# Kernel optimization log

Measured on AMD Instinct MI355X. Metric: run time of the kernel, lower is better.

Reference implementation:

```python
import jax, jax.numpy as jnp
import numpy as np

I = 1739   # input/output feature size (num_nodes)
H = 256    # hidden size
T = 2048   # trajectory length


def gru(x_seq, h0, W_ih, W_hh, b_ih, b_hh):
    """PyTorch-convention GRU over x_seq [T, I] with h0 [H]. Returns (hs [T,H], h_T [H])."""
    x_proj = x_seq @ W_ih.T + b_ih  # [T, 3H], precompute input projections

    def step(h, xp):
        hh = h @ W_hh.T + b_hh  # [3H]
        xr, xz, xn = xp[:H], xp[H:2 * H], xp[2 * H:]
        hr, hz, hn = hh[:H], hh[H:2 * H], hh[2 * H:]
        r = jax.nn.sigmoid(xr + hr)
        z = jax.nn.sigmoid(xz + hz)
        n = jnp.tanh(xn + r * hn)
        h_new = (1.0 - z) * n + z * h
        return h_new, h_new

    h_T, hs = jax.lax.scan(step, h0, x_proj)
    return hs, h_T


def setup_inputs() -> dict:
    key = jax.random.key(0)
    ks = jax.random.split(key, 12)
    s = 1.0 / np.sqrt(H)
    inp = {
        "input_trajectory": jax.random.normal(ks[0], (1, T, I), jnp.float32),
        "target_trajectory": jax.random.normal(ks[1], (1, T, I), jnp.float32),
        "W_ih_enc": jax.random.uniform(ks[2], (3 * H, I), jnp.float32, -s, s),
        "W_hh_enc": jax.random.uniform(ks[3], (3 * H, H), jnp.float32, -s, s),
        "b_ih_enc": jax.random.uniform(ks[4], (3 * H,), jnp.float32, -s, s),
        "b_hh_enc": jax.random.uniform(ks[5], (3 * H,), jnp.float32, -s, s),
        "W_ih_dec": jax.random.uniform(ks[6], (3 * H, I), jnp.float32, -s, s),
        "W_hh_dec": jax.random.uniform(ks[7], (3 * H, H), jnp.float32, -s, s),
        "b_ih_dec": jax.random.uniform(ks[8], (3 * H,), jnp.float32, -s, s),
        "b_hh_dec": jax.random.uniform(ks[9], (3 * H,), jnp.float32, -s, s),
        "W_out": jax.random.uniform(ks[10], (I, H), jnp.float32, -s, s),
        "b_out": jax.random.uniform(ks[11], (I,), jnp.float32, -s, s),
    }
    return inp


def reference(input_trajectory, target_trajectory,
              W_ih_enc, W_hh_enc, b_ih_enc, b_hh_enc,
              W_ih_dec, W_hh_dec, b_ih_dec, b_hh_dec,
              W_out, b_out):
    x = input_trajectory[0]  # [T, I], batch=1
    h0 = jnp.zeros((H,), x.dtype)
    # Encoder: only the final hidden state is used.
    _, h_enc = gru(x, h0, W_ih_enc, W_hh_enc, b_ih_enc, b_hh_enc)
    # Decoder: loop feeds each input timestep through a 1-step GRU;
    # this is exactly a GRU over the full sequence starting from h_enc.
    hs, _ = gru(x, h_enc, W_ih_dec, W_hh_dec, b_ih_dec, b_hh_dec)  # [T, H]
    # Per-step Linear is a single batched matmul over all steps.
    preds = hs @ W_out.T + b_out  # [T, I]
    # Original cats per-step (1,1,I) tensors along dim=0 -> [T, 1, I].
    return preds[:, None, :]
```

## Files before the change

kernel.cpp:

```cpp
#include <hip/hip_runtime.h>
#include <hip/hip_fp16.h>

#define TT 2048
#define II 1739
#define HN 256
#define H3 768

typedef _Float16 h2 __attribute__((ext_vector_type(2)));

__device__ __forceinline__ float fdot2(h2 a, h2 b, float c) {
#if defined(__has_builtin)
#if __has_builtin(__builtin_amdgcn_fdot2)
  return __builtin_amdgcn_fdot2(a, b, c, false);
#else
  return fmaf((float)a[0], (float)b[0], fmaf((float)a[1], (float)b[1], c));
#endif
#else
  return fmaf((float)a[0], (float)b[0], fmaf((float)a[1], (float)b[1], c));
#endif
}

template <int CTRL>
__device__ __forceinline__ float dpp_qperm(float v) {
  int r = __builtin_amdgcn_update_dpp(0, __builtin_bit_cast(int, v), CTRL, 0xF, 0xF, true);
  return __builtin_bit_cast(float, r);
}

__global__ __launch_bounds__(256) void gemm_abt(
    const float* __restrict__ A, int M, int K,
    const float* __restrict__ B, int N,
    const float* __restrict__ bias1, const float* __restrict__ bias2, int b2lim,
    float* __restrict__ C) {
  __shared__ float As[16][64];
  __shared__ float Bs[16][64];
  const int tid = threadIdx.x;
  const int m0 = blockIdx.y * 64, n0 = blockIdx.x * 64;
  const int lr = tid >> 2;
  const int lk = (tid & 3) * 4;
  const int cx = tid & 15, cy = tid >> 4;
  float acc[4][4] = {};

  for (int k0 = 0; k0 < K; k0 += 16) {
#pragma unroll
    for (int i = 0; i < 4; ++i) {
      int k = k0 + lk + i;
      As[lk + i][lr] = (k < K) ? A[(size_t)(m0 + lr) * K + k] : 0.f;
      int bn = n0 + lr;
      Bs[lk + i][lr] = (k < K && bn < N) ? B[(size_t)bn * K + k] : 0.f;
    }
    __syncthreads();
#pragma unroll
    for (int k = 0; k < 16; ++k) {
      float4 av = *(const float4*)&As[k][cy * 4];
      float4 bv = *(const float4*)&Bs[k][cx * 4];
      const float aa[4] = {av.x, av.y, av.z, av.w};
      const float bb[4] = {bv.x, bv.y, bv.z, bv.w};
#pragma unroll
      for (int i = 0; i < 4; ++i)
#pragma unroll
        for (int j = 0; j < 4; ++j) acc[i][j] = fmaf(aa[i], bb[j], acc[i][j]);
    }
    __syncthreads();
  }
#pragma unroll
  for (int i = 0; i < 4; ++i) {
    int m = m0 + cy * 4 + i;
#pragma unroll
    for (int j = 0; j < 4; ++j) {
      int n = n0 + cx * 4 + j;
      if (n < N) {
        float b = bias1 ? bias1[n] : 0.f;
        if (bias2 && n < b2lim) b += bias2[n];
        C[(size_t)m * N + n] = acc[i][j] + b;
      }
    }
  }
}

__global__ __launch_bounds__(512) void gru_seq(
    const float* __restrict__ xp,
    const float* __restrict__ Whh,
    const float* __restrict__ bhh,
    const float* __restrict__ h0,
    float* __restrict__ hs_out,
    float* __restrict__ hT_out) {
  __shared__ uint4 hbuf[32];
  __shared__ float hh[H3];

  const int tid = threadIdx.x;
  const int lane = tid & 63;
  const int wv = tid >> 6;
  const int kc = lane & 3;
  const int g = wv * 16 + (lane >> 2);
  const int r0 = g * 6;

  h2 wreg[6][32];
#pragma unroll
  for (int i = 0; i < 6; ++i) {
    const float* wr = Whh + (size_t)(r0 + i) * HN + kc * 64;
#pragma unroll
    for (int p = 0; p < 32; ++p) {
      float2 f = *(const float2*)(wr + 2 * p);
      wreg[i][p] = h2{(_Float16)f.x, (_Float16)f.y};
    }
  }

  float hj = 0.f, bhn = 0.f;
  if (tid < HN) {
    hj = h0 ? h0[tid] : 0.f;
    bhn = bhh[2 * HN + tid];
  }
  if (tid < 128) {
    float a = h0 ? h0[2 * tid] : 0.f;
    float b = h0 ? h0[2 * tid + 1] : 0.f;
    ((h2*)hbuf)[tid] = h2{(_Float16)a, (_Float16)b};
  }
  __syncthreads();

  for (int t = 0; t < TT; ++t) {
    float xr = 0.f, xz = 0.f, xn = 0.f;
    if (tid < HN) {
      const float* xpt = xp + (size_t)t * H3 + tid;
      xr = xpt[0];
      xz = xpt[HN];
      xn = xpt[2 * HN];
    }

    float acc[6] = {0.f, 0.f, 0.f, 0.f, 0.f, 0.f};
#pragma unroll
    for (int hf = 0; hf < 2; ++hf) {
      uint4 v0 = hbuf[kc * 8 + hf * 4 + 0];
      uint4 v1 = hbuf[kc * 8 + hf * 4 + 1];
      uint4 v2 = hbuf[kc * 8 + hf * 4 + 2];
      uint4 v3 = hbuf[kc * 8 + hf * 4 + 3];
      uint hw[16] = {v0.x, v0.y, v0.z, v0.w, v1.x, v1.y, v1.z, v1.w,
                     v2.x, v2.y, v2.z, v2.w, v3.x, v3.y, v3.z, v3.w};
#pragma unroll
      for (int i = 0; i < 6; ++i)
#pragma unroll
        for (int p = 0; p < 16; ++p)
          acc[i] = fdot2(wreg[i][hf * 16 + p], __builtin_bit_cast(h2, hw[p]), acc[i]);
    }

#pragma unroll
    for (int i = 0; i < 6; ++i) {
      float v = acc[i];
      v += dpp_qperm<0xB1>(v);
      v += dpp_qperm<0x4E>(v);
      acc[i] = v;
    }
    if (kc == 0) {
      *(float2*)&hh[r0 + 0] = make_float2(acc[0], acc[1]);
      *(float2*)&hh[r0 + 2] = make_float2(acc[2], acc[3]);
      *(float2*)&hh[r0 + 4] = make_float2(acc[4], acc[5]);
    }
    __syncthreads();

    if (tid < HN) {
      float r = 1.f / (1.f + __expf(-(xr + hh[tid])));
      float z = 1.f / (1.f + __expf(-(xz + hh[HN + tid])));
      float nv = 2.f / (1.f + __expf(-2.f * (xn + r * (hh[2 * HN + tid] + bhn)))) - 1.f;
      hj = (1.f - z) * nv + z * hj;
      if (hs_out) hs_out[(size_t)t * HN + tid] = hj;
      ((_Float16*)hbuf)[tid] = (_Float16)hj;
    }
    __syncthreads();
  }
  if (hT_out && tid < HN) hT_out[tid] = hj;
}

extern "C" void kernel_launch(void* const* d_in, const int* in_sizes, int n_in,
                              void* d_out, int out_size, void* d_ws, size_t ws_size,
                              hipStream_t stream) {
  const float* x     = (const float*)d_in[0];
  const float* Wih_e = (const float*)d_in[2];
  const float* Whh_e = (const float*)d_in[3];
  const float* bih_e = (const float*)d_in[4];
  const float* bhh_e = (const float*)d_in[5];
  const float* Wih_d = (const float*)d_in[6];
  const float* Whh_d = (const float*)d_in[7];
  const float* bih_d = (const float*)d_in[8];
  const float* bhh_d = (const float*)d_in[9];
  const float* Wout  = (const float*)d_in[10];
  const float* bout  = (const float*)d_in[11];
  float* out = (float*)d_out;

  float* ws = (float*)d_ws;
  float* xpe  = ws;
  float* xpd  = xpe + (size_t)TT * H3;
  float* hs   = xpd + (size_t)TT * H3;
  float* henc = hs + (size_t)TT * HN;

  dim3 blk(256);
  gemm_abt<<<dim3(12, 32), blk, 0, stream>>>(x, TT, II, Wih_e, H3, bih_e, bhh_e, 2 * HN, xpe);
  gemm_abt<<<dim3(12, 32), blk, 0, stream>>>(x, TT, II, Wih_d, H3, bih_d, bhh_d, 2 * HN, xpd);
  gru_seq<<<1, 512, 0, stream>>>(xpe, Whh_e, bhh_e, nullptr, nullptr, henc);
  gru_seq<<<1, 512, 0, stream>>>(xpd, Whh_d, bhh_d, henc, hs, nullptr);
  gemm_abt<<<dim3(28, 32), blk, 0, stream>>>(hs, TT, HN, Wout, II, bout, nullptr, 0, out);
}
```

Before: 5.527 ms.

## Fuse GRU gate math into dot-product threads with double-buffered h and one barrier

Each quad of lanes now owns two hidden units across all three gates, so the gate nonlinearities run right after the DPP reduction. This removes the shared hh buffer and one of the two barriers per timestep. The hidden-state buffer is double-buffered and padded to cut bank conflicts. The log2(e) scaling is folded into the input-projection GEMM and the recurrent weights so the gates can use raw exp2/rcp intrinsics. The cost is that fp16 weights now carry scaled values and more threads do redundant gate math.

```diff
diff --git a/kernel.cpp b/kernel.cpp
--- a/kernel.cpp
+++ b/kernel.cpp
@@ -5,6 +5,7 @@
 #define II 1739
 #define HN 256
 #define H3 768
+#define L2E 1.44269504088896f
 
 typedef _Float16 h2 __attribute__((ext_vector_type(2)));
 
@@ -20,6 +21,30 @@
 #endif
 }
 
+__device__ __forceinline__ float fast_exp2(float x) {
+#if defined(__has_builtin)
+#if __has_builtin(__builtin_amdgcn_exp2f)
+  return __builtin_amdgcn_exp2f(x);
+#else
+  return exp2f(x);
+#endif
+#else
+  return exp2f(x);
+#endif
+}
+
+__device__ __forceinline__ float fast_rcp(float x) {
+#if defined(__has_builtin)
+#if __has_builtin(__builtin_amdgcn_rcpf)
+  return __builtin_amdgcn_rcpf(x);
+#else
+  return 1.f / x;
+#endif
+#else
+  return 1.f / x;
+#endif
+}
+
 template <int CTRL>
 __device__ __forceinline__ float dpp_qperm(float v) {
   int r = __builtin_amdgcn_update_dpp(0, __builtin_bit_cast(int, v), CTRL, 0xF, 0xF, true);
@@ -30,6 +55,7 @@
     const float* __restrict__ A, int M, int K,
     const float* __restrict__ B, int N,
     const float* __restrict__ bias1, const float* __restrict__ bias2, int b2lim,
+    float s_lo, float s_hi, int slim,
     float* __restrict__ C) {
   __shared__ float As[16][64];
   __shared__ float Bs[16][64];
@@ -71,7 +97,8 @@
       if (n < N) {
         float b = bias1 ? bias1[n] : 0.f;
         if (bias2 && n < b2lim) b += bias2[n];
-        C[(size_t)m * N + n] = acc[i][j] + b;
+        float s = (n < slim) ? s_lo : s_hi;
+        C[(size_t)m * N + n] = (acc[i][j] + b) * s;
       }
     }
   }
@@ -84,89 +111,90 @@
     const float* __restrict__ h0,
     float* __restrict__ hs_out,
     float* __restrict__ hT_out) {
-  __shared__ uint4 hbuf[32];
-  __shared__ float hh[H3];
+  __shared__ __align__(16) uint hbufd[2][160];
 
   const int tid = threadIdx.x;
   const int lane = tid & 63;
   const int wv = tid >> 6;
   const int kc = lane & 3;
-  const int g = wv * 16 + (lane >> 2);
-  const int r0 = g * 6;
+  const int q = wv * 16 + (lane >> 2);
+  const int u0 = 2 * q;
 
   h2 wreg[6][32];
 #pragma unroll
-  for (int i = 0; i < 6; ++i) {
-    const float* wr = Whh + (size_t)(r0 + i) * HN + kc * 64;
-#pragma unroll
-    for (int p = 0; p < 32; ++p) {
-      float2 f = *(const float2*)(wr + 2 * p);
-      wreg[i][p] = h2{(_Float16)f.x, (_Float16)f.y};
-    }
-  }
-
-  float hj = 0.f, bhn = 0.f;
-  if (tid < HN) {
-    hj = h0 ? h0[tid] : 0.f;
-    bhn = bhh[2 * HN + tid];
-  }
+  for (int uu = 0; uu < 2; ++uu) {
+#pragma unroll
+    for (int gg = 0; gg < 3; ++gg) {
+      const float sc = (gg == 2) ? (2.f * L2E) : L2E;
+      const float* wr = Whh + (size_t)(u0 + uu + gg * HN) * HN + kc * 64;
+#pragma unroll
+      for (int p = 0; p < 32; ++p) {
+        float2 f = *(const float2*)(wr + 2 * p);
+        wreg[uu * 3 + gg][p] = h2{(_Float16)(f.x * sc), (_Float16)(f.y * sc)};
+      }
+    }
+  }
+
+  float hj0 = h0 ? h0[u0] : 0.f;
+  float hj1 = h0 ? h0[u0 + 1] : 0.f;
+  const float bhn0 = bhh[2 * HN + u0] * (2.f * L2E);
+  const float bhn1 = bhh[2 * HN + u0 + 1] * (2.f * L2E);
+
   if (tid < 128) {
     float a = h0 ? h0[2 * tid] : 0.f;
     float b = h0 ? h0[2 * tid + 1] : 0.f;
-    ((h2*)hbuf)[tid] = h2{(_Float16)a, (_Float16)b};
+    h2 pv = h2{(_Float16)a, (_Float16)b};
+    hbufd[0][(tid >> 5) * 40 + (tid & 31)] = __builtin_bit_cast(uint, pv);
   }
   __syncthreads();
 
+  const float* xpt = xp + u0;
+  const int wadr = (q >> 5) * 40 + (q & 31);
+
   for (int t = 0; t < TT; ++t) {
-    float xr = 0.f, xz = 0.f, xn = 0.f;
-    if (tid < HN) {
-      const float* xpt = xp + (size_t)t * H3 + tid;
-      xr = xpt[0];
-      xz = xpt[HN];
-      xn = xpt[2 * HN];
-    }
-
-    float acc[6] = {0.f, 0.f, 0.f, 0.f, 0.f, 0.f};
-#pragma unroll
-    for (int hf = 0; hf < 2; ++hf) {
-      uint4 v0 = hbuf[kc * 8 + hf * 4 + 0];
-      uint4 v1 = hbuf[kc * 8 + hf * 4 + 1];
-      uint4 v2 = hbuf[kc * 8 + hf * 4 + 2];
-      uint4 v3 = hbuf[kc * 8 + hf * 4 + 3];
-      uint hw[16] = {v0.x, v0.y, v0.z, v0.w, v1.x, v1.y, v1.z, v1.w,
-                     v2.x, v2.y, v2.z, v2.w, v3.x, v3.y, v3.z, v3.w};
+    float2 xr = *(const float2*)(xpt);
+    float2 xz = *(const float2*)(xpt + HN);
+    float2 xn = *(const float2*)(xpt + 2 * HN);
+    xpt += H3;
+
+    const uint* hb = &hbufd[t & 1][kc * 40];
+    float a[6] = {0.f, 0.f, 0.f, 0.f, 0.f, 0.f};
+#pragma unroll
+    for (int qq = 0; qq < 8; ++qq) {
+      uint4 v = *(const uint4*)&hb[qq * 4];
+      uint hwv[4] = {v.x, v.y, v.z, v.w};
 #pragma unroll
       for (int i = 0; i < 6; ++i)
 #pragma unroll
-        for (int p = 0; p < 16; ++p)
-          acc[i] = fdot2(wreg[i][hf * 16 + p], __builtin_bit_cast(h2, hw[p]), acc[i]);
+        for (int p = 0; p < 4; ++p)
+          a[i] = fdot2(wreg[i][qq * 4 + p], __builtin_bit_cast(h2, hwv[p]), a[i]);
     }
 
 #pragma unroll
     for (int i = 0; i < 6; ++i) {
-      float v = acc[i];
+      float v = a[i];
       v += dpp_qperm<0xB1>(v);
       v += dpp_qperm<0x4E>(v);
-      acc[i] = v;
-    }
+      a[i] = v;
+    }
+
+    float r0 = fast_rcp(1.f + fast_exp2(-(xr.x + a[0])));
+    float z0 = fast_rcp(1.f + fast_exp2(-(xz.x + a[1])));
+    float n0 = fmaf(2.f, fast_rcp(1.f + fast_exp2(-fmaf(r0, a[2] + bhn0, xn.x))), -1.f);
+    hj0 = fmaf(z0, hj0 - n0, n0);
+    float r1 = fast_rcp(1.f + fast_exp2(-(xr.y + a[3])));
+    float z1 = fast_rcp(1.f + fast_exp2(-(xz.y + a[4])));
+    float n1 = fmaf(2.f, fast_rcp(1.f + fast_exp2(-fmaf(r1, a[5] + bhn1, xn.y))), -1.f);
+    hj1 = fmaf(z1, hj1 - n1, n1);
+
+    h2 pv = h2{(_Float16)hj0, (_Float16)hj1};
     if (kc == 0) {
-      *(float2*)&hh[r0 + 0] = make_float2(acc[0], acc[1]);
-      *(float2*)&hh[r0 + 2] = make_float2(acc[2], acc[3]);
-      *(float2*)&hh[r0 + 4] = make_float2(acc[4], acc[5]);
+      hbufd[(t & 1) ^ 1][wadr] = __builtin_bit_cast(uint, pv);
+      if (hs_out) *(float2*)&hs_out[(size_t)t * HN + u0] = make_float2(hj0, hj1);
     }
     __syncthreads();
-
-    if (tid < HN) {
-      float r = 1.f / (1.f + __expf(-(xr + hh[tid])));
-      float z = 1.f / (1.f + __expf(-(xz + hh[HN + tid])));
-      float nv = 2.f / (1.f + __expf(-2.f * (xn + r * (hh[2 * HN + tid] + bhn)))) - 1.f;
-      hj = (1.f - z) * nv + z * hj;
-      if (hs_out) hs_out[(size_t)t * HN + tid] = hj;
-      ((_Float16*)hbuf)[tid] = (_Float16)hj;
-    }
-    __syncthreads();
-  }
-  if (hT_out && tid < HN) hT_out[tid] = hj;
+  }
+  if (hT_out && kc == 0) *(float2*)&hT_out[u0] = make_float2(hj0, hj1);
 }
 
 extern "C" void kernel_launch(void* const* d_in, const int* in_sizes, int n_in,
@@ -192,9 +220,12 @@
   float* henc = hs + (size_t)TT * HN;
 
   dim3 blk(256);
-  gemm_abt<<<dim3(12, 32), blk, 0, stream>>>(x, TT, II, Wih_e, H3, bih_e, bhh_e, 2 * HN, xpe);
-  gemm_abt<<<dim3(12, 32), blk, 0, stream>>>(x, TT, II, Wih_d, H3, bih_d, bhh_d, 2 * HN, xpd);
+  gemm_abt<<<dim3(12, 32), blk, 0, stream>>>(x, TT, II, Wih_e, H3, bih_e, bhh_e, 2 * HN,
+                                             L2E, 2.f * L2E, 2 * HN, xpe);
+  gemm_abt<<<dim3(12, 32), blk, 0, stream>>>(x, TT, II, Wih_d, H3, bih_d, bhh_d, 2 * HN,
+                                             L2E, 2.f * L2E, 2 * HN, xpd);
   gru_seq<<<1, 512, 0, stream>>>(xpe, Whh_e, bhh_e, nullptr, nullptr, henc);
   gru_seq<<<1, 512, 0, stream>>>(xpd, Whh_d, bhh_d, henc, hs, nullptr);
-  gemm_abt<<<dim3(28, 32), blk, 0, stream>>>(hs, TT, HN, Wout, II, bout, nullptr, 0, out);
-}
+  gemm_abt<<<dim3(28, 32), blk, 0, stream>>>(hs, TT, HN, Wout, II, bout, nullptr, 0,
+                                             1.f, 1.f, 0, out);
+}
```

Result: faster. 5.026 ms (-9.1%).
